# Kernel optimization log

Hardware: AMD Instinct MI355X
Metric: run time of the kernel (lower is better)

The kernel has to match this reference:

```python
import jax, jax.numpy as jnp
import numpy as np
import math

EMBED_DIM = 1024
NUM_HEADS = 16
HEAD_DIM = EMBED_DIM // NUM_HEADS
WINDOW_SIZE = 32  # one-sided; full window = 2*w+1 = 65
SCALING = math.sqrt(HEAD_DIM)


def setup_inputs() -> dict:
    key = jax.random.key(0)
    ks = jax.random.split(key, 9)
    B, S, E = 2, 2048, EMBED_DIM
    s = 1.0 / math.sqrt(E)
    inp = {
        "hidden_states": jax.random.normal(ks[0], (B, S, E), dtype=jnp.float32),
        "q_w": jax.random.uniform(ks[1], (E, E), jnp.float32, -s, s),
        "q_b": jax.random.uniform(ks[2], (E,), jnp.float32, -s, s),
        "k_w": jax.random.uniform(ks[3], (E, E), jnp.float32, -s, s),
        "k_b": jax.random.uniform(ks[4], (E,), jnp.float32, -s, s),
        "v_w": jax.random.uniform(ks[5], (E, E), jnp.float32, -s, s),
        "v_b": jax.random.uniform(ks[6], (E,), jnp.float32, -s, s),
        "o_w": jax.random.uniform(ks[7], (E, E), jnp.float32, -s, s),
        "o_b": jax.random.uniform(ks[8], (E,), jnp.float32, -s, s),
    }
    return inp


def reference(hidden_states, q_w, q_b, k_w, k_b, v_w, v_b, o_w, o_b):
    B, S, E = hidden_states.shape
    H, D, w = NUM_HEADS, HEAD_DIM, WINDOW_SIZE
    W = 2 * w + 1

    q = hidden_states @ q_w.T + q_b
    k = hidden_states @ k_w.T + k_b
    v = hidden_states @ v_w.T + v_b

    # [B, H, S, D]
    q = q.reshape(B, S, H, D).transpose(0, 2, 1, 3)
    k = k.reshape(B, S, H, D).transpose(0, 2, 1, 3)
    v = v.reshape(B, S, H, D).transpose(0, 2, 1, 3)

    # zero-pad seq dim by w on each side (matches F.pad value=0); padded keys
    # contribute score 0 (NOT -inf) exactly like the original unfold scheme.
    k_pad = jnp.pad(k, ((0, 0), (0, 0), (w, w), (0, 0)))
    v_pad = jnp.pad(v, ((0, 0), (0, 0), (w, w), (0, 0)))

    # window gather indices: query i sees padded positions i..i+2w (orig i-w..i+w)
    idx = jnp.arange(S)[:, None] + jnp.arange(W)[None, :]  # [S, W]
    k_slice = k_pad[:, :, idx]  # [B, H, S, W, D]
    v_slice = v_pad[:, :, idx]  # [B, H, S, W, D]

    score = jnp.einsum('bhsd,bhswd->bhsw', q, k_slice) / SCALING
    p = jax.nn.softmax(score, axis=-1)
    attn = jnp.einsum('bhsw,bhswd->bhsd', p, v_slice)

    attn = attn.transpose(0, 2, 1, 3).reshape(B, S, E)
    return attn @ o_w.T + o_b
```

## Files before the change

### kernel.cpp

```cpp
#include <hip/hip_runtime.h>
#include <math.h>

typedef _Float16 h16;
typedef _Float16 h8 __attribute__((ext_vector_type(8)));
typedef float f32x4 __attribute__((ext_vector_type(4)));

__device__ inline void gl2lds16(const void* g, void* l) {
  __builtin_amdgcn_global_load_lds(
      (const __attribute__((address_space(1))) void*)g,
      (__attribute__((address_space(3))) void*)l, 16, 0, 0);
}

__device__ inline void barrier_raw() {
  asm volatile("" ::: "memory");
  __builtin_amdgcn_s_barrier();
  asm volatile("" ::: "memory");
}

#define VMCNT(N) asm volatile("s_waitcnt vmcnt(" #N ")" ::: "memory")

__global__ __launch_bounds__(256) void f2h_all(
    const float* __restrict__ hs, const float* __restrict__ w0,
    const float* __restrict__ w1, const float* __restrict__ w2,
    const float* __restrict__ w3, h16* __restrict__ dst, int hsN) {
  int i = (blockIdx.x * 256 + threadIdx.x) * 8;
  const int tot = hsN + 4 * 1048576;
  if (i >= tot) return;
  const float* src;
  int off;
  if (i < hsN) {
    src = hs; off = i;
  } else {
    int k = i - hsN;
    int seg = k >> 20;
    off = k & 1048575;
    src = seg == 0 ? w0 : seg == 1 ? w1 : seg == 2 ? w2 : w3;
  }
  float4 a = *(const float4*)(src + off);
  float4 b = *(const float4*)(src + off + 4);
  h8 o;
  o[0] = (h16)a.x; o[1] = (h16)a.y; o[2] = (h16)a.z; o[3] = (h16)a.w;
  o[4] = (h16)b.x; o[5] = (h16)b.y; o[6] = (h16)b.z; o[7] = (h16)b.w;
  *(h8*)(dst + i) = o;
}

__global__ __launch_bounds__(512, 2) void qkv8(
    const h16* __restrict__ A, const h16* __restrict__ Bw,
    const float* __restrict__ qb, const float* __restrict__ kb,
    const float* __restrict__ vb, h16* __restrict__ qo, h16* __restrict__ ko,
    h16* __restrict__ vo, int nbm, int cpx) {
  __shared__ __align__(16) h16 Asm[2][256][64];
  __shared__ __align__(16) h16 Bsm[2][256][64];

  const int tid = threadIdx.x;
  const int wid = tid >> 6, lane = tid & 63;
  const int lr = lane & 15, lg = lane >> 4;
  const int wr = wid >> 2, wc = wid & 3;
  const int srow = wid * 8 + (lane >> 3);
  const int lsrc = ((lane & 7) ^ (srow & 7)) * 8;

  const int wg = (blockIdx.x % 8) * cpx + blockIdx.x / 8;
  const int bm = wg % nbm, bn = wg / nbm;
  const int row0 = bm * 256, col0 = bn * 256;

  const h16* Ag = A + (size_t)row0 * 1024;
  const h16* Bg = Bw + (size_t)col0 * 1024;

  auto stg = [&](const h16* g, h16* l, int rs) {
    gl2lds16(g + (size_t)(rs + srow) * 1024 + lsrc, l + (rs + wid * 8) * 64);
  };
  auto ldf = [&](const h16* base, int row, int kk) -> h8 {
    return *(const h8*)(base + row * 64 + ((kk * 4 + lg) ^ (lr & 7)) * 8);
  };

  f32x4 acc[8][4] = {};

  stg(Bg, &Bsm[0][0][0], 0);   stg(Bg, &Bsm[0][0][0], 64);
  stg(Bg, &Bsm[0][0][0], 128); stg(Bg, &Bsm[0][0][0], 192);
  stg(Ag, &Asm[0][0][0], 0);   stg(Ag, &Asm[0][0][0], 128);
  stg(Ag, &Asm[0][0][0], 64);  stg(Ag, &Asm[0][0][0], 192);
  VMCNT(2);
  barrier_raw();

  h8 bf[4][2], af[2][2];

#define MMA16(MG)                                                              \
  __builtin_amdgcn_s_setprio(1);                                               \
  _Pragma("unroll") for (int kk = 0; kk < 2; ++kk)                             \
      _Pragma("unroll") for (int mi = 0; mi < 2; ++mi)                         \
          _Pragma("unroll") for (int n = 0; n < 4; ++n)                        \
              acc[(MG)*2 + mi][n] = __builtin_amdgcn_mfma_f32_16x16x32_f16(    \
                  af[mi][kk], bf[n][kk], acc[(MG)*2 + mi][n], 0, 0, 0);        \
  __builtin_amdgcn_s_setprio(0)

  for (int t = 0; t < 16; ++t) {
    const int buf = t & 1;
    const h16* Ar = &Asm[buf][0][0];
    const h16* Br = &Bsm[buf][0][0];
    h16* Aw = &Asm[buf ^ 1][0][0];
    h16* Bww = &Bsm[buf ^ 1][0][0];
    const h16* Agt = Ag + (t + 1) * 64;
    const h16* Bgt = Bg + (t + 1) * 64;
    const bool st = (t < 15);

#pragma unroll
    for (int n = 0; n < 4; ++n) {
      bf[n][0] = ldf(Br, wc * 64 + n * 16 + lr, 0);
      bf[n][1] = ldf(Br, wc * 64 + n * 16 + lr, 1);
    }
#pragma unroll
    for (int kk = 0; kk < 2; ++kk) {
      af[0][kk] = ldf(Ar, wr * 128 + 0 * 16 + lr, kk);
      af[1][kk] = ldf(Ar, wr * 128 + 1 * 16 + lr, kk);
    }
    if (st) { stg(Bgt, Bww, 0); stg(Bgt, Bww, 64); }
    barrier_raw();
    MMA16(0);
    barrier_raw();

#pragma unroll
    for (int kk = 0; kk < 2; ++kk) {
      af[0][kk] = ldf(Ar, wr * 128 + 2 * 16 + lr, kk);
      af[1][kk] = ldf(Ar, wr * 128 + 3 * 16 + lr, kk);
    }
    if (st) { stg(Bgt, Bww, 128); stg(Bgt, Bww, 192); }
    barrier_raw();
    MMA16(1);
    if (st) { VMCNT(4); } else { VMCNT(0); }
    barrier_raw();

#pragma unroll
    for (int kk = 0; kk < 2; ++kk) {
      af[0][kk] = ldf(Ar, wr * 128 + 4 * 16 + lr, kk);
      af[1][kk] = ldf(Ar, wr * 128 + 5 * 16 + lr, kk);
    }
    if (st) { stg(Agt, Aw, 0); stg(Agt, Aw, 128); }
    barrier_raw();
    MMA16(2);
    barrier_raw();

#pragma unroll
    for (int kk = 0; kk < 2; ++kk) {
      af[0][kk] = ldf(Ar, wr * 128 + 6 * 16 + lr, kk);
      af[1][kk] = ldf(Ar, wr * 128 + 7 * 16 + lr, kk);
    }
    if (st) { stg(Agt, Aw, 64); stg(Agt, Aw, 192); }
    barrier_raw();
    MMA16(3);
    if (st) { VMCNT(2); } else { VMCNT(0); }
    barrier_raw();
  }
#undef MMA16

  const int tsel = col0 >> 10;
  const float* bp = tsel == 0 ? qb : (tsel == 1 ? kb : vb);
  h16* outp = tsel == 0 ? qo : (tsel == 1 ? ko : vo);
#pragma unroll
  for (int n = 0; n < 4; ++n) {
    const int cidx = col0 + wc * 64 + n * 16 + lr;
    const int jj = cidx & 1023;
    const float bv = bp[jj];
    const int hh = jj >> 6, dd = jj & 63;
#pragma unroll
    for (int m = 0; m < 8; ++m) {
#pragma unroll
      for (int j = 0; j < 4; ++j) {
        const int r = row0 + wr * 128 + m * 16 + lg * 4 + j;
        const int bb = r >> 11, ss = r & 2047;
        outp[(((size_t)bb * 16 + hh) * 2048 + ss) * 64 + dd] =
            (h16)(acc[m][n][j] + bv);
      }
    }
  }
}

__global__ __launch_bounds__(256) void gemm_o(
    const h16* __restrict__ A, const h16* __restrict__ Bw,
    const float* __restrict__ b0, float* __restrict__ Cf, int M, int N, int K) {
  __shared__ __align__(16) h16 Ash[128 * 32];
  __shared__ __align__(16) h16 Bsh[128 * 32];
  const int tid = threadIdx.x;
  const int wave = tid >> 6, lane = tid & 63;
  const int lr = lane & 15, lg = lane >> 4;
  const int wr = wave >> 1, wc = wave & 1;
  const int row0 = blockIdx.x * 128, col0 = blockIdx.y * 128;

  f32x4 acc[4][4] = {};

  const int nk = K >> 5;
  for (int kt = 0; kt < nk; ++kt) {
#pragma unroll
    for (int i = 0; i < 2; ++i) {
      const int grp = wave * 2 + i;
      const int c = grp * 64 + lane;
      const int r = c >> 2, cc = c & 3;
      gl2lds16(A + (size_t)(row0 + r) * K + kt * 32 + cc * 8, &Ash[grp * 512]);
      gl2lds16(Bw + (size_t)(col0 + r) * K + kt * 32 + cc * 8, &Bsh[grp * 512]);
    }
    __syncthreads();
    h8 af[4], bf[4];
#pragma unroll
    for (int m = 0; m < 4; ++m)
      af[m] = *(const h8*)&Ash[(wr * 64 + m * 16 + lr) * 32 + lg * 8];
#pragma unroll
    for (int n = 0; n < 4; ++n)
      bf[n] = *(const h8*)&Bsh[(wc * 64 + n * 16 + lr) * 32 + lg * 8];
#pragma unroll
    for (int m = 0; m < 4; ++m)
#pragma unroll
      for (int n = 0; n < 4; ++n)
        acc[m][n] =
            __builtin_amdgcn_mfma_f32_16x16x32_f16(af[m], bf[n], acc[m][n], 0, 0, 0);
    __syncthreads();
  }

#pragma unroll
  for (int m = 0; m < 4; ++m)
#pragma unroll
    for (int n = 0; n < 4; ++n)
#pragma unroll
      for (int j = 0; j < 4; ++j) {
        const int r = row0 + wr * 64 + m * 16 + lg * 4 + j;
        const int cidx = col0 + wc * 64 + n * 16 + lr;
        Cf[(size_t)r * N + cidx] = acc[m][n][j] + b0[cidx];
      }
}

__global__ __launch_bounds__(256) void swattn(const h16* __restrict__ Q,
                                              const h16* __restrict__ K,
                                              const h16* __restrict__ V,
                                              h16* __restrict__ O) {
  __shared__ __align__(16) h16 Ksh[128 * 72];
  __shared__ __align__(16) h16 Vsh[64 * 136];
  __shared__ __align__(16) h16 Psh[4][16 * 136];

  const int qb0 = blockIdx.x * 64;
  const int bh = blockIdx.y;
  const int b = bh >> 4, h = bh & 15;
  const int tid = threadIdx.x;
  const int wave = tid >> 6, lane = tid & 63;
  const int lr = lane & 15, lg = lane >> 4;

  const h16* Qb = Q + (size_t)bh * 2048 * 64;
  const h16* Kb = K + (size_t)bh * 2048 * 64;
  const h16* Vb = V + (size_t)bh * 2048 * 64;

#pragma unroll
  for (int i = 0; i < 4; ++i) {
    const int c = tid * 4 + i;
    const int row = c >> 3, c8 = c & 7;
    const int t = qb0 - 32 + row;
    h8 kv, vv;
    if (t >= 0 && t < 2048) {
      kv = *(const h8*)&Kb[(size_t)t * 64 + c8 * 8];
      vv = *(const h8*)&Vb[(size_t)t * 64 + c8 * 8];
    } else {
#pragma unroll
      for (int j = 0; j < 8; ++j) { kv[j] = (h16)0.f; vv[j] = (h16)0.f; }
    }
    *(h8*)&Ksh[row * 72 + c8 * 8] = kv;
#pragma unroll
    for (int j = 0; j < 8; ++j) Vsh[(c8 * 8 + j) * 136 + row] = vv[j];
  }
  __syncthreads();

  const int qrow = qb0 + wave * 16 + lr;
  h8 qa[2];
#pragma unroll
  for (int kk = 0; kk < 2; ++kk)
    qa[kk] = *(const h8*)&Qb[(size_t)qrow * 64 + kk * 32 + lg * 8];

  f32x4 sacc[8] = {};
#pragma unroll
  for (int n = 0; n < 8; ++n)
#pragma unroll
    for (int kk = 0; kk < 2; ++kk) {
      h8 kb = *(const h8*)&Ksh[(n * 16 + lr) * 72 + kk * 32 + lg * 8];
      sacc[n] = __builtin_amdgcn_mfma_f32_16x16x32_f16(qa[kk], kb, sacc[n], 0, 0, 0);
    }

  float p[8][4];
#pragma unroll
  for (int j = 0; j < 4; ++j) {
    const int wrow = wave * 16 + lg * 4 + j;
    float mx = -1e30f;
#pragma unroll
    for (int n = 0; n < 8; ++n) {
      const int d = n * 16 + lr - wrow;
      float s = (d < 0 || d > 64) ? -1e30f : sacc[n][j] * 0.125f;
      p[n][j] = s;
      mx = fmaxf(mx, s);
    }
#pragma unroll
    for (int off = 1; off < 16; off <<= 1) mx = fmaxf(mx, __shfl_xor(mx, off, 64));
    float sum = 0.f;
#pragma unroll
    for (int n = 0; n < 8; ++n) {
      const float e = __expf(p[n][j] - mx);
      p[n][j] = e;
      sum += e;
    }
#pragma unroll
    for (int off = 1; off < 16; off <<= 1) sum += __shfl_xor(sum, off, 64);
    const float inv = 1.f / sum;
#pragma unroll
    for (int n = 0; n < 8; ++n) p[n][j] *= inv;
  }

#pragma unroll
  for (int n = 0; n < 8; ++n)
#pragma unroll
    for (int j = 0; j < 4; ++j)
      Psh[wave][(lg * 4 + j) * 136 + n * 16 + lr] = (h16)p[n][j];
  __syncthreads();

  f32x4 oacc[4] = {};
#pragma unroll
  for (int kk = 0; kk < 4; ++kk) {
    h8 pa = *(const h8*)&Psh[wave][lr * 136 + kk * 32 + lg * 8];
#pragma unroll
    for (int n = 0; n < 4; ++n) {
      h8 vb = *(const h8*)&Vsh[(n * 16 + lr) * 136 + kk * 32 + lg * 8];
      oacc[n] = __builtin_amdgcn_mfma_f32_16x16x32_f16(pa, vb, oacc[n], 0, 0, 0);
    }
  }

#pragma unroll
  for (int n = 0; n < 4; ++n)
#pragma unroll
    for (int j = 0; j < 4; ++j) {
      const int s = qb0 + wave * 16 + lg * 4 + j;
      const int d = n * 16 + lr;
      O[((size_t)b * 2048 + s) * 1024 + h * 64 + d] = (h16)oacc[n][j];
    }
}

extern "C" void kernel_launch(void* const* d_in, const int* in_sizes, int n_in,
                              void* d_out, int out_size, void* d_ws, size_t ws_size,
                              hipStream_t stream) {
  const float* hs = (const float*)d_in[0];
  const float* qw = (const float*)d_in[1];
  const float* qb = (const float*)d_in[2];
  const float* kw = (const float*)d_in[3];
  const float* kb = (const float*)d_in[4];
  const float* vw = (const float*)d_in[5];
  const float* vb = (const float*)d_in[6];
  const float* ow = (const float*)d_in[7];
  const float* ob = (const float*)d_in[8];

  const int M = in_sizes[0] / 1024;

  h16* hsH = (h16*)d_ws;
  h16* wqkv = hsH + (size_t)M * 1024;
  h16* woH = wqkv + (size_t)3072 * 1024;
  h16* qH = woH + (size_t)1024 * 1024;
  h16* kH = qH + (size_t)M * 1024;
  h16* vH = kH + (size_t)M * 1024;
  h16* attnH = vH + (size_t)M * 1024;

  const int tot = M * 1024 + 4 * 1048576;
  f2h_all<<<(tot / 8 + 255) / 256, 256, 0, stream>>>(hs, qw, kw, vw, ow, hsH,
                                                     M * 1024);

  const int nbm = M / 256;
  const int nwg = nbm * 12;
  qkv8<<<nwg, 512, 0, stream>>>(hsH, wqkv, qb, kb, vb, qH, kH, vH, nbm, nwg / 8);

  swattn<<<dim3(32, M / 2048 * 16), 256, 0, stream>>>(qH, kH, vH, attnH);

  gemm_o<<<dim3(M / 128, 8), 256, 0, stream>>>(attnH, woH, ob, (float*)d_out, M,
                                               1024, 1024);
}
```

Measured before the change: 89.08 us.

## Double-buffer A fragments and reorder stage loads in QKV GEMM main loop

The QKV projection GEMM main loop now keeps two sets of A-operand register fragments, so the LDS reads for the next MFMA group are issued before the current group runs. Explicit lgkmcnt waits replace the implicit full waits. The global-to-LDS staging order is changed to load A rows first, and the loop is unrolled by two with constant buffer indices. The aim is to hide LDS read latency behind MFMA work and reduce barrier-exposed stalls. In exchange it raises register pressure and depends on the hand-set wait counts being correct for the reordered VMEM and LDS traffic.

Result: slower. 91.64 us (+2.9%).

```diff
diff --git a/kernel.cpp b/kernel.cpp
--- a/kernel.cpp
+++ b/kernel.cpp
@@ -18,6 +18,7 @@
 }
 
 #define VMCNT(N) asm volatile("s_waitcnt vmcnt(" #N ")" ::: "memory")
+#define LGKM(N) asm volatile("s_waitcnt lgkmcnt(" #N ")" ::: "memory")
 
 __global__ __launch_bounds__(256) void f2h_all(
     const float* __restrict__ hs, const float* __restrict__ w0,
@@ -74,83 +75,87 @@
   };
 
   f32x4 acc[8][4] = {};
-
+  h8 bf[4][2], afA[2][2], afB[2][2];
+
+  stg(Ag, &Asm[0][0][0], 0);   stg(Ag, &Asm[0][0][0], 128);
   stg(Bg, &Bsm[0][0][0], 0);   stg(Bg, &Bsm[0][0][0], 64);
   stg(Bg, &Bsm[0][0][0], 128); stg(Bg, &Bsm[0][0][0], 192);
-  stg(Ag, &Asm[0][0][0], 0);   stg(Ag, &Asm[0][0][0], 128);
   stg(Ag, &Asm[0][0][0], 64);  stg(Ag, &Asm[0][0][0], 192);
   VMCNT(2);
   barrier_raw();
 
-  h8 bf[4][2], af[2][2];
-
-#define MMA16(MG)                                                              \
+#define MMA2(AF, M0)                                                           \
   __builtin_amdgcn_s_setprio(1);                                               \
   _Pragma("unroll") for (int kk = 0; kk < 2; ++kk)                             \
       _Pragma("unroll") for (int mi = 0; mi < 2; ++mi)                         \
           _Pragma("unroll") for (int n = 0; n < 4; ++n)                        \
-              acc[(MG)*2 + mi][n] = __builtin_amdgcn_mfma_f32_16x16x32_f16(    \
-                  af[mi][kk], bf[n][kk], acc[(MG)*2 + mi][n], 0, 0, 0);        \
+              acc[(M0) + mi][n] = __builtin_amdgcn_mfma_f32_16x16x32_f16(      \
+                  AF[mi][kk], bf[n][kk], acc[(M0) + mi][n], 0, 0, 0);          \
   __builtin_amdgcn_s_setprio(0)
 
-  for (int t = 0; t < 16; ++t) {
-    const int buf = t & 1;
-    const h16* Ar = &Asm[buf][0][0];
-    const h16* Br = &Bsm[buf][0][0];
-    h16* Aw = &Asm[buf ^ 1][0][0];
-    h16* Bww = &Bsm[buf ^ 1][0][0];
-    const h16* Agt = Ag + (t + 1) * 64;
-    const h16* Bgt = Bg + (t + 1) * 64;
-    const bool st = (t < 15);
-
-#pragma unroll
-    for (int n = 0; n < 4; ++n) {
-      bf[n][0] = ldf(Br, wc * 64 + n * 16 + lr, 0);
-      bf[n][1] = ldf(Br, wc * 64 + n * 16 + lr, 1);
-    }
-#pragma unroll
-    for (int kk = 0; kk < 2; ++kk) {
-      af[0][kk] = ldf(Ar, wr * 128 + 0 * 16 + lr, kk);
-      af[1][kk] = ldf(Ar, wr * 128 + 1 * 16 + lr, kk);
-    }
-    if (st) { stg(Bgt, Bww, 0); stg(Bgt, Bww, 64); }
-    barrier_raw();
-    MMA16(0);
-    barrier_raw();
-
-#pragma unroll
-    for (int kk = 0; kk < 2; ++kk) {
-      af[0][kk] = ldf(Ar, wr * 128 + 2 * 16 + lr, kk);
-      af[1][kk] = ldf(Ar, wr * 128 + 3 * 16 + lr, kk);
-    }
-    if (st) { stg(Bgt, Bww, 128); stg(Bgt, Bww, 192); }
-    barrier_raw();
-    MMA16(1);
-    if (st) { VMCNT(4); } else { VMCNT(0); }
-    barrier_raw();
-
-#pragma unroll
-    for (int kk = 0; kk < 2; ++kk) {
-      af[0][kk] = ldf(Ar, wr * 128 + 4 * 16 + lr, kk);
-      af[1][kk] = ldf(Ar, wr * 128 + 5 * 16 + lr, kk);
-    }
-    if (st) { stg(Agt, Aw, 0); stg(Agt, Aw, 128); }
-    barrier_raw();
-    MMA16(2);
-    barrier_raw();
-
-#pragma unroll
-    for (int kk = 0; kk < 2; ++kk) {
-      af[0][kk] = ldf(Ar, wr * 128 + 6 * 16 + lr, kk);
-      af[1][kk] = ldf(Ar, wr * 128 + 7 * 16 + lr, kk);
-    }
-    if (st) { stg(Agt, Aw, 64); stg(Agt, Aw, 192); }
-    barrier_raw();
-    MMA16(3);
-    if (st) { VMCNT(2); } else { VMCNT(0); }
-    barrier_raw();
-  }
-#undef MMA16
+#define TILE_PHASES(T, RBUF, WBUF)                                             \
+  {                                                                            \
+    const h16* Ar = &Asm[RBUF][0][0];                                          \
+    const h16* Br = &Bsm[RBUF][0][0];                                          \
+    h16* Aw = &Asm[WBUF][0][0];                                                \
+    h16* Bwl = &Bsm[WBUF][0][0];                                               \
+    const h16* Agt = Ag + (size_t)((T) + 1) * 64;                              \
+    const h16* Bgt = Bg + (size_t)((T) + 1) * 64;                              \
+    const bool st = (T) < 15;                                                  \
+                             \
+    _Pragma("unroll") for (int n = 0; n < 4; ++n) {                            \
+      bf[n][0] = ldf(Br, wc * 64 + n * 16 + lr, 0);                            \
+      bf[n][1] = ldf(Br, wc * 64 + n * 16 + lr, 1);                            \
+    }                                                                          \
+    _Pragma("unroll") for (int kk = 0; kk < 2; ++kk) {                         \
+      afA[0][kk] = ldf(Ar, wr * 128 + 0 * 16 + lr, kk);                        \
+      afA[1][kk] = ldf(Ar, wr * 128 + 1 * 16 + lr, kk);                        \
+    }                                                                          \
+    _Pragma("unroll") for (int kk = 0; kk < 2; ++kk) {                         \
+      afB[0][kk] = ldf(Ar, wr * 128 + 2 * 16 + lr, kk);                        \
+      afB[1][kk] = ldf(Ar, wr * 128 + 3 * 16 + lr, kk);                        \
+    }                                                                          \
+    if (st) { stg(Agt, Aw, 0); stg(Agt, Aw, 128); }                            \
+    barrier_raw();                                                             \
+    LGKM(4);                                                                   \
+    MMA2(afA, 0);                                                              \
+    if (st) { VMCNT(2); } else { VMCNT(0); }                                   \
+    barrier_raw();                                                             \
+                                         \
+    _Pragma("unroll") for (int kk = 0; kk < 2; ++kk) {                         \
+      afA[0][kk] = ldf(Ar, wr * 128 + 4 * 16 + lr, kk);                        \
+      afA[1][kk] = ldf(Ar, wr * 128 + 5 * 16 + lr, kk);                        \
+    }                                                                          \
+    if (st) { stg(Bgt, Bwl, 0); stg(Bgt, Bwl, 64); }                           \
+    barrier_raw();                                                             \
+    LGKM(4);                                                                   \
+    MMA2(afB, 2);                                                              \
+    barrier_raw();                                                             \
+                                         \
+    _Pragma("unroll") for (int kk = 0; kk < 2; ++kk) {                         \
+      afB[0][kk] = ldf(Ar, wr * 128 + 6 * 16 + lr, kk);                        \
+      afB[1][kk] = ldf(Ar, wr * 128 + 7 * 16 + lr, kk);                        \
+    }                                                                          \
+    if (st) { stg(Bgt, Bwl, 128); stg(Bgt, Bwl, 192); }                        \
+    barrier_raw();                                                             \
+    LGKM(4);                                                                   \
+    MMA2(afA, 4);                                                              \
+    barrier_raw();                                                             \
+                                          \
+    if (st) { stg(Agt, Aw, 64); stg(Agt, Aw, 192); }                           \
+    barrier_raw();                                                             \
+    LGKM(0);                                                                   \
+    MMA2(afB, 6);                                                              \
+    if (st) { VMCNT(2); } else { VMCNT(0); }                                   \
+    barrier_raw();                                                             \
+  }
+
+  for (int tt = 0; tt < 16; tt += 2) {
+    TILE_PHASES(tt, 0, 1);
+    TILE_PHASES(tt + 1, 1, 0);
+  }
+#undef TILE_PHASES
+#undef MMA2
 
   const int tsel = col0 >> 10;
   const float* bp = tsel == 0 ? qb : (tsel == 1 ? kb : vb);
```
